# Kernel optimization log

Hardware: AMD Instinct MI355X
Metric: run time of the kernel (lower is better)

Reference implementation:

```python
import jax, jax.numpy as jnp
import numpy as np

NL, D, ED, N, K, DT_RANK, V, L, B = 24, 768, 1536, 16, 4, 48, 1024, 512, 2


def setup_inputs() -> dict:
    key = jax.random.key(0)
    ks = jax.random.split(key, 12)
    s = 0.02
    rn = lambda k, shape: jax.random.normal(k, shape, dtype=jnp.float32) * s
    return {
        "src": jax.random.randint(ks[0], (L, B), 0, V),
        "embed": rn(ks[1], (V, D)),
        "norm_w": jnp.ones((NL, D), jnp.float32),
        "in_proj": rn(ks[2], (NL, 2 * ED, D)),
        "conv_w": rn(ks[3], (NL, ED, K)) * 10.0,  # ~N(0, 0.2)
        "conv_b": jnp.zeros((NL, ED), jnp.float32),
        "x_proj": rn(ks[4], (NL, DT_RANK + 2 * N, ED)),
        "dt_w": rn(ks[5], (NL, ED, DT_RANK)),
        # softplus(dt_b) in ~[0.007, 0.05], like HF Mamba's dt init range
        "dt_b": jax.random.uniform(ks[6], (NL, ED), minval=-5.0, maxval=-3.0),
        # S4D-real init: A = -[1..N]
        "A_log": jnp.log(jnp.broadcast_to(jnp.arange(1, N + 1, dtype=jnp.float32), (NL, ED, N))),
        "Dp": jnp.ones((NL, ED), jnp.float32),
        "out_proj": rn(ks[7], (NL, D, ED)),
        "normf_w": jnp.ones((D,), jnp.float32),
    }


def _rmsnorm(x, w, eps=1e-5):
    return x * jax.lax.rsqrt(jnp.mean(x * x, axis=-1, keepdims=True) + eps) * w


def _forward(src, embed, norm_w, in_proj, conv_w, conv_b, x_proj, dt_w, dt_b,
             A_log, Dp, out_proj, normf_w):
    ids = src.T  # [B, L] (module does src.T.contiguous())
    h = embed[ids]  # [B, L, D]

    def layer(x, p):
        nw, W_in, cw, cb, W_x, W_dt, b_dt, a_log, d, W_out = p
        ug = jnp.einsum('bld,ed->ble', _rmsnorm(x, nw), W_in)  # [B,L,2ED]
        u, g = jnp.split(ug, 2, axis=-1)
        # depthwise causal conv1d, kernel K
        up = jnp.pad(u, ((0, 0), (K - 1, 0), (0, 0)))
        uc = sum(up[:, k:k + u.shape[1], :] * cw[:, k] for k in range(K)) + cb
        uc = jax.nn.silu(uc)
        # SSM parameters
        sp = jnp.einsum('ble,se->bls', uc, W_x)
        dt_r, Bm, Cm = jnp.split(sp, [DT_RANK, DT_RANK + N], axis=-1)
        dt = jax.nn.softplus(jnp.einsum('blr,er->ble', dt_r, W_dt) + b_dt)  # [B,L,ED]
        A = -jnp.exp(a_log)  # [ED, N]

        def step(hst, ins):
            dt_t, B_t, C_t, u_t = ins  # [B,ED],[B,N],[B,N],[B,ED]
            dA = jnp.exp(dt_t[..., None] * A)            # [B,ED,N]
            hst = dA * hst + (dt_t * u_t)[..., None] * B_t[:, None, :]
            y = jnp.einsum('ben,bn->be', hst, C_t)
            return hst, y

        h0 = jnp.zeros((x.shape[0], ED, N), x.dtype)
        xs = (dt.transpose(1, 0, 2), Bm.transpose(1, 0, 2),
              Cm.transpose(1, 0, 2), uc.transpose(1, 0, 2))
        _, ys = jax.lax.scan(step, h0, xs)                # [L,B,ED]
        y = ys.transpose(1, 0, 2) + uc * d
        y = y * jax.nn.silu(g)
        return x + jnp.einsum('ble,de->bld', y, W_out), None

    h, _ = jax.lax.scan(layer, h, (norm_w, in_proj, conv_w, conv_b, x_proj,
                                   dt_w, dt_b, A_log, Dp, out_proj))
    h = _rmsnorm(h, normf_w)
    logits = jnp.einsum('bld,vd->blv', h, embed)  # tied lm_head, no bias
    return logits.transpose(1, 0, 2)  # [L, B, V] (module returns x.transpose(0,1))


def reference(src, embed, norm_w, in_proj, conv_w, conv_b, x_proj, dt_w, dt_b,
              A_log, Dp, out_proj, normf_w):
    return _forward(src, embed, norm_w, in_proj, conv_w, conv_b, x_proj, dt_w,
                    dt_b, A_log, Dp, out_proj, normf_w)
```

## Files before the change

### kernel.cpp

```cpp
#include <hip/hip_runtime.h>
#include <hip/hip_bf16.h>
#include <math.h>

#define NL   24
#define DDIM 768
#define ED   1536
#define NST  16
#define KC   4
#define DTR  48
#define VV   1024
#define LL   512
#define BB   2
#define MM   (BB*LL)
#define SP   80

#define NC   32
#define CL   (LL/NC)

#define XKS  32
#define XKC  (ED/XKS)

#define OPS  4
#define OPK  (ED/OPS)

typedef unsigned short u16;
typedef __bf16 bf16x8 __attribute__((ext_vector_type(8)));
typedef float  floatx4 __attribute__((ext_vector_type(4)));
typedef unsigned short ushort4v __attribute__((ext_vector_type(4)));

typedef const __attribute__((address_space(1))) void gvoid_t;
typedef __attribute__((address_space(3))) void svoid_t;

#define GLD16(g, l) __builtin_amdgcn_global_load_lds((gvoid_t*)(g), (svoid_t*)(l), 16, 0, 0)

__device__ __forceinline__ float softplusf(float x) {
    return fmaxf(x, 0.0f) + log1pf(__expf(-fabsf(x)));
}
__device__ __forceinline__ float siluf(float x) {
    return x / (1.0f + __expf(-x));
}
__device__ __forceinline__ u16 f2bf(float x) {
    unsigned int u = __builtin_bit_cast(unsigned int, x);
    u += 0x7FFFu + ((u >> 16) & 1u);
    return (u16)(u >> 16);
}

__global__ __launch_bounds__(256) void cvt_bf16_kernel(
        const float* __restrict__ in, u16* __restrict__ out, int n4)
{
    int stride = gridDim.x * 256;
    for (int i = blockIdx.x * 256 + threadIdx.x; i < n4; i += stride) {
        float4 v = reinterpret_cast<const float4*>(in)[i];
        ushort4v o = {f2bf(v.x), f2bf(v.y), f2bf(v.z), f2bf(v.w)};
        reinterpret_cast<ushort4v*>(out)[i] = o;
    }
}

__global__ __launch_bounds__(256) void embed_kernel(
        const int* __restrict__ src, const float* __restrict__ emb,
        float* __restrict__ h)
{
    int m = blockIdx.x;
    int b = m >> 9;
    int l = m & (LL - 1);
    int v = src[l * BB + b];
    const float* er = emb + (size_t)v * DDIM;
    float* hr = h + (size_t)m * DDIM;
    for (int d = threadIdx.x; d < DDIM; d += 256) hr[d] = er[d];
}

__global__ __launch_bounds__(256) void rmsnorm_kernel(
        const float* __restrict__ h, const float* __restrict__ w,
        u16* __restrict__ o)
{
    __shared__ float red[4];
    int m = blockIdx.x, tid = threadIdx.x;
    const float* hr = h + (size_t)m * DDIM;
    float v0 = hr[tid], v1 = hr[tid + 256], v2 = hr[tid + 512];
    float s = v0 * v0 + v1 * v1 + v2 * v2;
    #pragma unroll
    for (int off = 32; off; off >>= 1) s += __shfl_down(s, off);
    if ((tid & 63) == 0) red[tid >> 6] = s;
    __syncthreads();
    float tot = red[0] + red[1] + red[2] + red[3];
    float scale = rsqrtf(tot * (1.0f / DDIM) + 1e-5f);
    u16* orow = o + (size_t)m * DDIM;
    orow[tid]       = f2bf(v0 * scale * w[tid]);
    orow[tid + 256] = f2bf(v1 * scale * w[tid + 256]);
    orow[tid + 512] = f2bf(v2 * scale * w[tid + 512]);
}

template<int BNF, int MODE>
__global__ __launch_bounds__(256) void gemm_bf16_d(
        const u16* __restrict__ A, int lda,
        const u16* __restrict__ W, int ldb,
        float* __restrict__ C, int ldc,
        int Kper)
{
    __shared__ __attribute__((aligned(16))) u16 As[2][128 * 64];
    __shared__ __attribute__((aligned(16))) u16 Bs[2][BNF * 32 * 64];
    int tid  = threadIdx.x;
    int lane = tid & 63;
    int wave = tid >> 6;
    int wm = wave >> 1, wn = wave & 1;
    int colBase = blockIdx.x * (BNF * 32);
    int rowBase = blockIdx.y * 128;
    int k0 = blockIdx.z * Kper;

    floatx4 acc[4][BNF];
    #pragma unroll
    for (int i = 0; i < 4; i++)
        #pragma unroll
        for (int j = 0; j < BNF; j++)
            acc[i][j] = (floatx4){0.f, 0.f, 0.f, 0.f};

    int kc = lane >> 4;
    int lm = lane & 15;

    const u16* Ap[4];
    #pragma unroll
    for (int j = 0; j < 4; j++) {
        int q = (wave * 4 + j) * 64 + lane;
        int r = q >> 3, cg = (q & 7) ^ (r & 7);
        Ap[j] = A + (size_t)(rowBase + r) * lda + k0 + cg * 8;
    }
    const u16* Wp[BNF];
    #pragma unroll
    for (int j = 0; j < BNF; j++) {
        int q = (wave * BNF + j) * 64 + lane;
        int r = q >> 3, cg = (q & 7) ^ (r & 7);
        Wp[j] = W + (size_t)(colBase + r) * ldb + k0 + cg * 8;
    }

    auto stage = [&](int buf, int kk) {
        u16* as = &As[buf][0];
        u16* bs = &Bs[buf][0];
        #pragma unroll
        for (int j = 0; j < 4; j++) GLD16(Ap[j] + kk, as + (wave * 4 + j) * 512);
        #pragma unroll
        for (int j = 0; j < BNF; j++) GLD16(Wp[j] + kk, bs + (wave * BNF + j) * 512);
    };

    int nt = Kper >> 6;
    stage(0, 0);
    __syncthreads();
    for (int t = 0; t < nt; t++) {
        int cur = t & 1;
        if (t + 1 < nt) stage(cur ^ 1, (t + 1) * 64);
        #pragma unroll
        for (int ks = 0; ks < 2; ks++) {
            int ck = ks * 4 + kc;
            bf16x8 af[4], bw[BNF];
            #pragma unroll
            for (int i = 0; i < 4; i++) {
                int m = wm * 64 + i * 16 + lm;
                af[i] = *reinterpret_cast<const bf16x8*>(
                    &As[cur][m * 64 + ((ck ^ (m & 7)) * 8)]);
            }
            #pragma unroll
            for (int j = 0; j < BNF; j++) {
                int n = wn * (BNF * 16) + j * 16 + lm;
                bw[j] = *reinterpret_cast<const bf16x8*>(
                    &Bs[cur][n * 64 + ((ck ^ (n & 7)) * 8)]);
            }
            #pragma unroll
            for (int i = 0; i < 4; i++)
                #pragma unroll
                for (int j = 0; j < BNF; j++)
                    acc[i][j] = __builtin_amdgcn_mfma_f32_16x16x32_bf16(
                        af[i], bw[j], acc[i][j], 0, 0, 0);
        }
        __syncthreads();
    }

    int c4 = (lane >> 4) * 4;
    #pragma unroll
    for (int i = 0; i < 4; i++) {
        #pragma unroll
        for (int j = 0; j < BNF; j++) {
            floatx4 v = acc[i][j];
            int col = colBase + wn * (BNF * 16) + j * 16 + lm;
            #pragma unroll
            for (int p = 0; p < 4; p++) {
                int row = rowBase + wm * 64 + i * 16 + c4 + p;
                if (MODE == 3) {
                    int l = row & (LL - 1), b = row >> 9;
                    C[((size_t)l * BB + b) * ldc + col] = v[p];
                } else if (MODE == 5) {
                    atomicAdd(&C[(size_t)row * ldc + col], v[p]);
                } else {
                    C[(size_t)row * ldc + col] = v[p];
                }
            }
        }
    }
}

__global__ __launch_bounds__(256) void sgemm_nt(
        const float* __restrict__ A, int lda,
        const float* __restrict__ W, int ldb,
        float* __restrict__ C, int ldc,
        int Nmat, int Kdim, int mode, const float* __restrict__ bias)
{
    __shared__ float As[16][65];
    __shared__ float Ws[16][65];
    int tid = threadIdx.x;
    int tx = tid & 15, ty = tid >> 4;
    int rowBase = blockIdx.x * 64;
    int colBase = blockIdx.y * 64;
    float acc[4][4] = {};

    for (int kk = 0; kk < Kdim; kk += 16) {
        #pragma unroll
        for (int i = 0; i < 4; i++) {
            int idx = tid + i * 256;
            int r = idx >> 4, kc = idx & 15;
            As[kc][r] = A[(size_t)(rowBase + r) * lda + kk + kc];
            int cG = colBase + r;
            Ws[kc][r] = (cG < Nmat) ? W[(size_t)cG * ldb + kk + kc] : 0.0f;
        }
        __syncthreads();
        #pragma unroll
        for (int k = 0; k < 16; k++) {
            float av[4], bv[4];
            #pragma unroll
            for (int i = 0; i < 4; i++) av[i] = As[k][ty + 16 * i];
            #pragma unroll
            for (int j = 0; j < 4; j++) bv[j] = Ws[k][tx + 16 * j];
            #pragma unroll
            for (int i = 0; i < 4; i++)
                #pragma unroll
                for (int j = 0; j < 4; j++)
                    acc[i][j] = fmaf(av[i], bv[j], acc[i][j]);
        }
        __syncthreads();
    }

    #pragma unroll
    for (int i = 0; i < 4; i++) {
        int m = rowBase + ty + 16 * i;
        #pragma unroll
        for (int j = 0; j < 4; j++) {
            int n = colBase + tx + 16 * j;
            if (n >= Nmat) continue;
            float v = acc[i][j];
            if (mode == 0) {
                C[(size_t)m * ldc + n] = v;
            } else {
                C[(size_t)m * ldc + n] = softplusf(v + bias[n]);
            }
        }
    }
}

__global__ __launch_bounds__(256) void xproj_conv_partial(
        const float* __restrict__ ug, const float* __restrict__ cw,
        const float* __restrict__ cb, const float* __restrict__ W,
        float* __restrict__ part, float* __restrict__ ucb)
{
    __shared__ float As[16][65];
    __shared__ float Ws[16][88];
    int tid = threadIdx.x;
    int tx = tid & 15;
    int ty = tid >> 4;
    int rowBase = blockIdx.x * 64;
    int k0 = blockIdx.y * XKC;
    float acc[4][5] = {};

    for (int kk = 0; kk < XKC; kk += 16) {
        #pragma unroll
        for (int i = 0; i < 4; i++) {
            int idx = tid + i * 256;
            int r = idx >> 4, kc = idx & 15;
            int m = rowBase + r;
            int e = k0 + kk + kc;
            int b = m >> 9, l = m & (LL - 1);
            float a = cb[e];
            #pragma unroll
            for (int k = 0; k < KC; k++) {
                int ll = l + k - (KC - 1);
                float uv = (ll >= 0) ? ug[((size_t)(b * LL + ll)) * (2 * ED) + e] : 0.0f;
                a = fmaf(uv, cw[e * KC + k], a);
            }
            a = siluf(a);
            As[kc][r] = a;
            ucb[(size_t)m * ED + e] = a;
        }
        #pragma unroll
        for (int i = 0; i < 5; i++) {
            int idx = tid + i * 256;
            int c = idx >> 4, kc = idx & 15;
            Ws[kc][c] = W[(size_t)c * ED + k0 + kk + kc];
        }
        __syncthreads();
        #pragma unroll
        for (int k = 0; k < 16; k++) {
            float av[4], bv[5];
            #pragma unroll
            for (int i = 0; i < 4; i++) av[i] = As[k][ty + 16 * i];
            #pragma unroll
            for (int j = 0; j < 5; j++) bv[j] = Ws[k][tx + 16 * j];
            #pragma unroll
            for (int i = 0; i < 4; i++)
                #pragma unroll
                for (int j = 0; j < 5; j++)
                    acc[i][j] = fmaf(av[i], bv[j], acc[i][j]);
        }
        __syncthreads();
    }

    float* p = part + ((size_t)blockIdx.y * MM + rowBase) * SP;
    #pragma unroll
    for (int i = 0; i < 4; i++)
        #pragma unroll
        for (int j = 0; j < 5; j++)
            p[(ty + 16 * i) * SP + tx + 16 * j] = acc[i][j];
}

__global__ __launch_bounds__(256) void xproj_reduce(
        const float* __restrict__ part, float* __restrict__ spb)
{
    int idx = blockIdx.x * 256 + threadIdx.x;
    float4 s = {0.f, 0.f, 0.f, 0.f};
    #pragma unroll
    for (int ks = 0; ks < XKS; ks++) {
        float4 v = reinterpret_cast<const float4*>(part + (size_t)ks * MM * SP)[idx];
        s.x += v.x; s.y += v.y; s.z += v.z; s.w += v.w;
    }
    reinterpret_cast<float4*>(spb)[idx] = s;
}

__global__ __launch_bounds__(256) void scan_pass1(
        const float* __restrict__ dtb, const float* __restrict__ ucb,
        const float* __restrict__ spb, const float* __restrict__ A_log,
        float* __restrict__ hfin, float* __restrict__ sumdt)
{
    int e = blockIdx.x * 256 + threadIdx.x;
    int c = blockIdx.y;
    int b = blockIdx.z;
    float a[NST], h[NST];
    const float4* ap = reinterpret_cast<const float4*>(A_log + (size_t)e * NST);
    #pragma unroll
    for (int q = 0; q < 4; q++) {
        float4 v = ap[q];
        a[4*q+0] = -__expf(v.x); a[4*q+1] = -__expf(v.y);
        a[4*q+2] = -__expf(v.z); a[4*q+3] = -__expf(v.w);
    }
    #pragma unroll
    for (int n = 0; n < NST; n++) h[n] = 0.0f;
    float sdt = 0.0f;
    int m0 = b * LL + c * CL;
    for (int l = 0; l < CL; l++) {
        int m = m0 + l;
        float dtv = dtb[(size_t)m * ED + e];
        float ucv = ucb[(size_t)m * ED + e];
        const float4* bp = reinterpret_cast<const float4*>(spb + (size_t)m * SP + DTR);
        float x = dtv * ucv;
        sdt += dtv;
        #pragma unroll
        for (int q = 0; q < 4; q++) {
            float4 bv = bp[q];
            h[4*q+0] = fmaf(__expf(dtv * a[4*q+0]), h[4*q+0], x * bv.x);
            h[4*q+1] = fmaf(__expf(dtv * a[4*q+1]), h[4*q+1], x * bv.y);
            h[4*q+2] = fmaf(__expf(dtv * a[4*q+2]), h[4*q+2], x * bv.z);
            h[4*q+3] = fmaf(__expf(dtv * a[4*q+3]), h[4*q+3], x * bv.w);
        }
    }
    float* hf = hfin + (((size_t)(b * ED + e)) * NC + c) * NST;
    #pragma unroll
    for (int n = 0; n < NST; n++) hf[n] = h[n];
    sumdt[((size_t)(b * ED + e)) * NC + c] = sdt;
}

__global__ __launch_bounds__(256) void scan_mid(
        const float* __restrict__ hfin, const float* __restrict__ sumdt,
        const float* __restrict__ A_log, float* __restrict__ hstart)
{
    int gid = blockIdx.x * 256 + threadIdx.x;
    int n = gid & 15;
    int be = gid >> 4;
    int e = be % ED;
    float a = -__expf(A_log[(size_t)e * NST + n]);
    float h = 0.0f;
    const float* hf = hfin + (size_t)be * NC * NST;
    const float* sd = sumdt + (size_t)be * NC;
    float* hs = hstart + (size_t)be * NC * NST;
    for (int c = 0; c < NC; c++) {
        hs[c * NST + n] = h;
        h = fmaf(__expf(a * sd[c]), h, hf[c * NST + n]);
    }
}

__global__ __launch_bounds__(256) void scan_pass2(
        const float* __restrict__ dtb, const float* __restrict__ ucb,
        const float* __restrict__ spb, const float* __restrict__ ugb,
        const float* __restrict__ A_log, const float* __restrict__ Dp,
        const float* __restrict__ hstart, u16* __restrict__ yb)
{
    int e = blockIdx.x * 256 + threadIdx.x;
    int c = blockIdx.y;
    int b = blockIdx.z;
    float a[NST], h[NST];
    const float4* ap = reinterpret_cast<const float4*>(A_log + (size_t)e * NST);
    #pragma unroll
    for (int q = 0; q < 4; q++) {
        float4 v = ap[q];
        a[4*q+0] = -__expf(v.x); a[4*q+1] = -__expf(v.y);
        a[4*q+2] = -__expf(v.z); a[4*q+3] = -__expf(v.w);
    }
    const float* hs = hstart + (((size_t)(b * ED + e)) * NC + c) * NST;
    #pragma unroll
    for (int n = 0; n < NST; n++) h[n] = hs[n];
    float dpv = Dp[e];
    int m0 = b * LL + c * CL;
    for (int l = 0; l < CL; l++) {
        int m = m0 + l;
        float dtv = dtb[(size_t)m * ED + e];
        float ucv = ucb[(size_t)m * ED + e];
        const float4* bp = reinterpret_cast<const float4*>(spb + (size_t)m * SP + DTR);
        const float4* cp = reinterpret_cast<const float4*>(spb + (size_t)m * SP + DTR + NST);
        float g = ugb[(size_t)m * (2 * ED) + ED + e];
        float x = dtv * ucv;
        float y0 = 0.0f, y1 = 0.0f, y2 = 0.0f, y3 = 0.0f;
        #pragma unroll
        for (int q = 0; q < 4; q++) {
            float4 bv = bp[q];
            float4 cv = cp[q];
            h[4*q+0] = fmaf(__expf(dtv * a[4*q+0]), h[4*q+0], x * bv.x);
            h[4*q+1] = fmaf(__expf(dtv * a[4*q+1]), h[4*q+1], x * bv.y);
            h[4*q+2] = fmaf(__expf(dtv * a[4*q+2]), h[4*q+2], x * bv.z);
            h[4*q+3] = fmaf(__expf(dtv * a[4*q+3]), h[4*q+3], x * bv.w);
            y0 = fmaf(h[4*q+0], cv.x, y0);
            y1 = fmaf(h[4*q+1], cv.y, y1);
            y2 = fmaf(h[4*q+2], cv.z, y2);
            y3 = fmaf(h[4*q+3], cv.w, y3);
        }
        float yv = (y0 + y1) + (y2 + y3) + ucv * dpv;
        yb[(size_t)m * ED + e] = f2bf(yv * siluf(g));
    }
}

extern "C" void kernel_launch(void* const* d_in, const int* in_sizes, int n_in,
                              void* d_out, int out_size, void* d_ws, size_t ws_size,
                              hipStream_t stream) {
    const int*   src    = (const int*)  d_in[0];
    const float* emb    = (const float*)d_in[1];
    const float* norm_w = (const float*)d_in[2];
    const float* in_prj = (const float*)d_in[3];
    const float* conv_w = (const float*)d_in[4];
    const float* conv_b = (const float*)d_in[5];
    const float* x_prj  = (const float*)d_in[6];
    const float* dt_w   = (const float*)d_in[7];
    const float* dt_b   = (const float*)d_in[8];
    const float* A_log  = (const float*)d_in[9];
    const float* Dp     = (const float*)d_in[10];
    const float* out_p  = (const float*)d_in[11];
    const float* normf  = (const float*)d_in[12];
    float* out = (float*)d_out;

    float* ws    = (float*)d_ws;
    float* h     = ws;
    float* xn_f  = h     + (size_t)MM * DDIM;
    float* ug    = xn_f  + (size_t)MM * DDIM;
    float* ucb   = ug    + (size_t)MM * 2 * ED;
    float* spb   = ucb   + (size_t)MM * ED;
    float* dtbf  = spb   + (size_t)MM * SP;
    float* yb_f  = dtbf  + (size_t)MM * ED;
    float* hfin  = yb_f  + (size_t)MM * ED;
    float* sumdt = hfin  + (size_t)BB * ED * NC * NST;
    float* hstart= sumdt + (size_t)BB * ED * NC;
    float* wend  = hstart+ (size_t)BB * ED * NC * NST;

    u16* xn = (u16*)xn_f;
    u16* yb = (u16*)yb_f;
    u16* wbf_in  = (u16*)wend;
    u16* wbf_out = wbf_in  + (size_t)NL * 2 * ED * DDIM;
    u16* wbf_emb = wbf_out + (size_t)NL * DDIM * ED;
    float* xpart = (float*)(wbf_emb + (size_t)VV * DDIM);

    cvt_bf16_kernel<<<2048, 256, 0, stream>>>(in_prj, wbf_in, NL * 2 * ED * DDIM / 4);
    cvt_bf16_kernel<<<2048, 256, 0, stream>>>(out_p, wbf_out, NL * DDIM * ED / 4);
    cvt_bf16_kernel<<<256, 256, 0, stream>>>(emb, wbf_emb, VV * DDIM / 4);

    embed_kernel<<<MM, 256, 0, stream>>>(src, emb, h);

    for (int layer = 0; layer < NL; layer++) {
        rmsnorm_kernel<<<MM, 256, 0, stream>>>(
            h, norm_w + (size_t)layer * DDIM, xn);
        gemm_bf16_d<2, 0><<<dim3(2 * ED / 64, MM / 128, 1), 256, 0, stream>>>(
            xn, DDIM, wbf_in + (size_t)layer * 2 * ED * DDIM, DDIM,
            ug, 2 * ED, DDIM);
        xproj_conv_partial<<<dim3(MM / 64, XKS), 256, 0, stream>>>(
            ug, conv_w + (size_t)layer * ED * KC, conv_b + (size_t)layer * ED,
            x_prj + (size_t)layer * SP * ED, xpart, ucb);
        xproj_reduce<<<MM * SP / 1024, 256, 0, stream>>>(xpart, spb);
        sgemm_nt<<<dim3(MM / 64, ED / 64), 256, 0, stream>>>(
            spb, SP, dt_w + (size_t)layer * ED * DTR, DTR,
            dtbf, ED, ED, DTR, 1, dt_b + (size_t)layer * ED);
        scan_pass1<<<dim3(ED / 256, NC, BB), 256, 0, stream>>>(
            dtbf, ucb, spb, A_log + (size_t)layer * ED * NST, hfin, sumdt);
        scan_mid<<<BB * ED * NST / 256, 256, 0, stream>>>(
            hfin, sumdt, A_log + (size_t)layer * ED * NST, hstart);
        scan_pass2<<<dim3(ED / 256, NC, BB), 256, 0, stream>>>(
            dtbf, ucb, spb, ug, A_log + (size_t)layer * ED * NST,
            Dp + (size_t)layer * ED, hstart, yb);
        gemm_bf16_d<2, 5><<<dim3(DDIM / 64, MM / 128, OPS), 256, 0, stream>>>(
            yb, ED, wbf_out + (size_t)layer * DDIM * ED, ED,
            h, DDIM, OPK);
    }

    rmsnorm_kernel<<<MM, 256, 0, stream>>>(h, normf, xn);
    gemm_bf16_d<1, 3><<<dim3(VV / 32, MM / 128, 1), 256, 0, stream>>>(
        xn, DDIM, wbf_emb, DDIM, out, VV, DDIM);
}
```

Measured before the change: 2.887 ms.

## Use atomic split-K accumulation for x_proj and fold chunk-carry scan into pass2

The separate xproj_reduce kernel is gone: split-K partial results of the x_proj GEMM are atomically added into a per-layer spb buffer, which one zero kernel clears up front for all layers. The scan_mid kernel is also gone, so each scan_pass2 block recomputes its starting state by serially combining the preceding chunks' final states and dt sums. This saves two launches per layer and the partial-buffer round trip. The cost is atomic contention (32 adds per element), non-deterministic summation order, and redundant carry work that grows with the chunk index (up to 31 steps of 16 exps).

```diff
diff --git a/kernel.cpp b/kernel.cpp
--- a/kernel.cpp
+++ b/kernel.cpp
@@ -56,6 +56,15 @@
     }
 }
 
+__global__ __launch_bounds__(256) void zero_kernel(
+        float* __restrict__ p, int n4)
+{
+    int stride = gridDim.x * 256;
+    float4 z = {0.f, 0.f, 0.f, 0.f};
+    for (int i = blockIdx.x * 256 + threadIdx.x; i < n4; i += stride)
+        reinterpret_cast<float4*>(p)[i] = z;
+}
+
 __global__ __launch_bounds__(256) void embed_kernel(
         const int* __restrict__ src, const float* __restrict__ emb,
         float* __restrict__ h)
@@ -256,7 +265,7 @@
 __global__ __launch_bounds__(256) void xproj_conv_partial(
         const float* __restrict__ ug, const float* __restrict__ cw,
         const float* __restrict__ cb, const float* __restrict__ W,
-        float* __restrict__ part, float* __restrict__ ucb)
+        float* __restrict__ spb, float* __restrict__ ucb)
 {
     __shared__ float As[16][65];
     __shared__ float Ws[16][88];
@@ -309,25 +318,12 @@
         __syncthreads();
     }
 
-    float* p = part + ((size_t)blockIdx.y * MM + rowBase) * SP;
     #pragma unroll
     for (int i = 0; i < 4; i++)
         #pragma unroll
         for (int j = 0; j < 5; j++)
-            p[(ty + 16 * i) * SP + tx + 16 * j] = acc[i][j];
-}
-
-__global__ __launch_bounds__(256) void xproj_reduce(
-        const float* __restrict__ part, float* __restrict__ spb)
-{
-    int idx = blockIdx.x * 256 + threadIdx.x;
-    float4 s = {0.f, 0.f, 0.f, 0.f};
-    #pragma unroll
-    for (int ks = 0; ks < XKS; ks++) {
-        float4 v = reinterpret_cast<const float4*>(part + (size_t)ks * MM * SP)[idx];
-        s.x += v.x; s.y += v.y; s.z += v.z; s.w += v.w;
-    }
-    reinterpret_cast<float4*>(spb)[idx] = s;
+            atomicAdd(&spb[(size_t)(rowBase + ty + 16 * i) * SP + tx + 16 * j],
+                      acc[i][j]);
 }
 
 __global__ __launch_bounds__(256) void scan_pass1(
@@ -372,30 +368,12 @@
     sumdt[((size_t)(b * ED + e)) * NC + c] = sdt;
 }
 
-__global__ __launch_bounds__(256) void scan_mid(
-        const float* __restrict__ hfin, const float* __restrict__ sumdt,
-        const float* __restrict__ A_log, float* __restrict__ hstart)
-{
-    int gid = blockIdx.x * 256 + threadIdx.x;
-    int n = gid & 15;
-    int be = gid >> 4;
-    int e = be % ED;
-    float a = -__expf(A_log[(size_t)e * NST + n]);
-    float h = 0.0f;
-    const float* hf = hfin + (size_t)be * NC * NST;
-    const float* sd = sumdt + (size_t)be * NC;
-    float* hs = hstart + (size_t)be * NC * NST;
-    for (int c = 0; c < NC; c++) {
-        hs[c * NST + n] = h;
-        h = fmaf(__expf(a * sd[c]), h, hf[c * NST + n]);
-    }
-}
-
 __global__ __launch_bounds__(256) void scan_pass2(
         const float* __restrict__ dtb, const float* __restrict__ ucb,
         const float* __restrict__ spb, const float* __restrict__ ugb,
         const float* __restrict__ A_log, const float* __restrict__ Dp,
-        const float* __restrict__ hstart, u16* __restrict__ yb)
+        const float* __restrict__ hfin, const float* __restrict__ sumdt,
+        u16* __restrict__ yb)
 {
     int e = blockIdx.x * 256 + threadIdx.x;
     int c = blockIdx.y;
@@ -408,9 +386,25 @@
         a[4*q+0] = -__expf(v.x); a[4*q+1] = -__expf(v.y);
         a[4*q+2] = -__expf(v.z); a[4*q+3] = -__expf(v.w);
     }
-    const float* hs = hstart + (((size_t)(b * ED + e)) * NC + c) * NST;
-    #pragma unroll
-    for (int n = 0; n < NST; n++) h[n] = hs[n];
+    #pragma unroll
+    for (int n = 0; n < NST; n++) h[n] = 0.0f;
+    {
+        size_t be = (size_t)(b * ED + e);
+        const float* sd = sumdt + be * NC;
+        const float* hfp = hfin + be * NC * NST;
+        for (int cp = 0; cp < c; cp++) {
+            float f = sd[cp];
+            const float4* hq = reinterpret_cast<const float4*>(hfp + cp * NST);
+            #pragma unroll
+            for (int q = 0; q < 4; q++) {
+                float4 hv = hq[q];
+                h[4*q+0] = fmaf(__expf(a[4*q+0] * f), h[4*q+0], hv.x);
+                h[4*q+1] = fmaf(__expf(a[4*q+1] * f), h[4*q+1], hv.y);
+                h[4*q+2] = fmaf(__expf(a[4*q+2] * f), h[4*q+2], hv.z);
+                h[4*q+3] = fmaf(__expf(a[4*q+3] * f), h[4*q+3], hv.w);
+            }
+        }
+    }
     float dpv = Dp[e];
     int m0 = b * LL + c * CL;
     for (int l = 0; l < CL; l++) {
@@ -418,14 +412,14 @@
         float dtv = dtb[(size_t)m * ED + e];
         float ucv = ucb[(size_t)m * ED + e];
         const float4* bp = reinterpret_cast<const float4*>(spb + (size_t)m * SP + DTR);
-        const float4* cp = reinterpret_cast<const float4*>(spb + (size_t)m * SP + DTR + NST);
+        const float4* cp4 = reinterpret_cast<const float4*>(spb + (size_t)m * SP + DTR + NST);
         float g = ugb[(size_t)m * (2 * ED) + ED + e];
         float x = dtv * ucv;
         float y0 = 0.0f, y1 = 0.0f, y2 = 0.0f, y3 = 0.0f;
         #pragma unroll
         for (int q = 0; q < 4; q++) {
             float4 bv = bp[q];
-            float4 cv = cp[q];
+            float4 cv = cp4[q];
             h[4*q+0] = fmaf(__expf(dtv * a[4*q+0]), h[4*q+0], x * bv.x);
             h[4*q+1] = fmaf(__expf(dtv * a[4*q+1]), h[4*q+1], x * bv.y);
             h[4*q+2] = fmaf(__expf(dtv * a[4*q+2]), h[4*q+2], x * bv.z);
@@ -463,28 +457,28 @@
     float* xn_f  = h     + (size_t)MM * DDIM;
     float* ug    = xn_f  + (size_t)MM * DDIM;
     float* ucb   = ug    + (size_t)MM * 2 * ED;
-    float* spb   = ucb   + (size_t)MM * ED;
-    float* dtbf  = spb   + (size_t)MM * SP;
+    float* spbA  = ucb   + (size_t)MM * ED;
+    float* dtbf  = spbA  + (size_t)NL * MM * SP;
     float* yb_f  = dtbf  + (size_t)MM * ED;
     float* hfin  = yb_f  + (size_t)MM * ED;
     float* sumdt = hfin  + (size_t)BB * ED * NC * NST;
-    float* hstart= sumdt + (size_t)BB * ED * NC;
-    float* wend  = hstart+ (size_t)BB * ED * NC * NST;
+    float* wend  = sumdt + (size_t)BB * ED * NC;
 
     u16* xn = (u16*)xn_f;
     u16* yb = (u16*)yb_f;
     u16* wbf_in  = (u16*)wend;
     u16* wbf_out = wbf_in  + (size_t)NL * 2 * ED * DDIM;
     u16* wbf_emb = wbf_out + (size_t)NL * DDIM * ED;
-    float* xpart = (float*)(wbf_emb + (size_t)VV * DDIM);
 
     cvt_bf16_kernel<<<2048, 256, 0, stream>>>(in_prj, wbf_in, NL * 2 * ED * DDIM / 4);
     cvt_bf16_kernel<<<2048, 256, 0, stream>>>(out_p, wbf_out, NL * DDIM * ED / 4);
     cvt_bf16_kernel<<<256, 256, 0, stream>>>(emb, wbf_emb, VV * DDIM / 4);
+    zero_kernel<<<512, 256, 0, stream>>>(spbA, NL * MM * SP / 4);
 
     embed_kernel<<<MM, 256, 0, stream>>>(src, emb, h);
 
     for (int layer = 0; layer < NL; layer++) {
+        float* spb = spbA + (size_t)layer * MM * SP;
         rmsnorm_kernel<<<MM, 256, 0, stream>>>(
             h, norm_w + (size_t)layer * DDIM, xn);
         gemm_bf16_d<2, 0><<<dim3(2 * ED / 64, MM / 128, 1), 256, 0, stream>>>(
@@ -492,18 +486,15 @@
             ug, 2 * ED, DDIM);
         xproj_conv_partial<<<dim3(MM / 64, XKS), 256, 0, stream>>>(
             ug, conv_w + (size_t)layer * ED * KC, conv_b + (size_t)layer * ED,
-            x_prj + (size_t)layer * SP * ED, xpart, ucb);
-        xproj_reduce<<<MM * SP / 1024, 256, 0, stream>>>(xpart, spb);
+            x_prj + (size_t)layer * SP * ED, spb, ucb);
         sgemm_nt<<<dim3(MM / 64, ED / 64), 256, 0, stream>>>(
             spb, SP, dt_w + (size_t)layer * ED * DTR, DTR,
             dtbf, ED, ED, DTR, 1, dt_b + (size_t)layer * ED);
         scan_pass1<<<dim3(ED / 256, NC, BB), 256, 0, stream>>>(
             dtbf, ucb, spb, A_log + (size_t)layer * ED * NST, hfin, sumdt);
-        scan_mid<<<BB * ED * NST / 256, 256, 0, stream>>>(
-            hfin, sumdt, A_log + (size_t)layer * ED * NST, hstart);
         scan_pass2<<<dim3(ED / 256, NC, BB), 256, 0, stream>>>(
             dtbf, ucb, spb, ug, A_log + (size_t)layer * ED * NST,
-            Dp + (size_t)layer * ED, hstart, yb);
+            Dp + (size_t)layer * ED, hfin, sumdt, yb);
         gemm_bf16_d<2, 5><<<dim3(DDIM / 64, MM / 128, OPS), 256, 0, stream>>>(
             yb, ED, wbf_out + (size_t)layer * DDIM * ED, ED,
             h, DDIM, OPK);
```

Measured after the change: 3.455 ms. 1.2x slower.
